# Kernel optimization log

Hardware: AMD Instinct MI355X
Metric: run time of the kernel (lower is better)

Reference implementation:

```python
import jax, jax.numpy as jnp
import numpy as np
from jax import lax

RF, NLF, MESH, FUSION = 64, 16, 16, 64


def _conv3x3(x, w, b):
    # stride 1, pad 1, ksize 3 == SAME
    y = lax.conv_general_dilated(x, w, (1, 1), 'SAME',
                                 dimension_numbers=('NCHW', 'OIHW', 'NCHW'))
    return y + b[None, :, None, None]


def _bn(x, g, b, m, v, eps=1e-5):
    scale = g / jnp.sqrt(v + eps)
    return (x - m[None, :, None, None]) * scale[None, :, None, None] + b[None, :, None, None]


def _rct_block(x, w1, b1, g, be, m, v, w2, b2):
    # extra_conv=True: Conv -> BN -> SiLU -> Conv (all stride 1)
    h = jax.nn.silu(_bn(_conv3x3(x, w1, b1), g, be, m, v))
    return _conv3x3(h, w2, b2)


def setup_inputs():
    key = jax.random.key(0)
    ks = jax.random.split(key, 8)
    B, H, W = 4, 512, 512
    return {
        'feature': jax.random.normal(ks[0], (B, RF, H, W), jnp.float32),
        'p_low': jax.random.normal(ks[1], (B, FUSION, MESH + 1, MESH + 1), jnp.float32),
        'r_w1': jax.random.normal(ks[2], (FUSION, FUSION, 3, 3), jnp.float32) * 0.05,
        'r_b1': jnp.zeros((FUSION,), jnp.float32),
        'r_gamma': jnp.ones((FUSION,), jnp.float32),
        'r_beta': jnp.zeros((FUSION,), jnp.float32),
        'r_mean': jnp.zeros((FUSION,), jnp.float32),
        'r_var': jnp.ones((FUSION,), jnp.float32),
        'r_w2': jax.random.normal(ks[3], (RF * NLF, FUSION, 3, 3), jnp.float32) * 0.05,
        'r_b2': jnp.zeros((RF * NLF,), jnp.float32),
        't_w1': jax.random.normal(ks[4], (FUSION, FUSION, 3, 3), jnp.float32) * 0.05,
        't_b1': jnp.zeros((FUSION,), jnp.float32),
        't_gamma': jnp.ones((FUSION,), jnp.float32),
        't_beta': jnp.zeros((FUSION,), jnp.float32),
        't_mean': jnp.zeros((FUSION,), jnp.float32),
        't_var': jnp.ones((FUSION,), jnp.float32),
        't_w2': jax.random.normal(ks[5], (3 * NLF, FUSION, 3, 3), jnp.float32) * 0.05,
        't_b2': jnp.zeros((3 * NLF,), jnp.float32),
    }


def reference(feature, p_low, r_w1, r_b1, r_gamma, r_beta, r_mean, r_var, r_w2, r_b2,
              t_w1, t_b1, t_gamma, t_beta, t_mean, t_var, t_w2, t_b2):
    B, C, H, W = feature.shape
    M = MESH
    mh, mw = H // M, W // M  # H,W divisible by mesh_size -> pad_tensor is identity
    P = mh * mw

    r_l = _rct_block(p_low, r_w1, r_b1, r_gamma, r_beta, r_mean, r_var, r_w2, r_b2)  # [B, RF*NLF, M+1, M+1]
    t_l = _rct_block(p_low, t_w1, t_b1, t_gamma, t_beta, t_mean, t_var, t_w2, t_b2)  # [B, 3*NLF, M+1, M+1]

    # channel dim factors as (feat, nlf); corners concat along nlf axis in order
    # (i,j), (i,j+1), (i+1,j), (i+1,j+1) -> K = 4*NLF keys per tile
    rc = r_l.reshape(B, RF, NLF, M + 1, M + 1)
    rk = jnp.concatenate([rc[..., :M, :M], rc[..., :M, 1:],
                          rc[..., 1:, :M], rc[..., 1:, 1:]], axis=2)  # [B,RF,4NLF,M,M]
    tc = t_l.reshape(B, 3, NLF, M + 1, M + 1)
    tk = jnp.concatenate([tc[..., :M, :M], tc[..., :M, 1:],
                          tc[..., 1:, :M], tc[..., 1:, 1:]], axis=2)  # [B,3,4NLF,M,M]

    # split feature into tiles: [B, M, M, P, RF] (row-major pixel order within tile)
    f = feature.reshape(B, RF, M, mh, M, mw).transpose(0, 2, 4, 3, 5, 1).reshape(B, M, M, P, RF)

    scale = 1.0 / jnp.sqrt(jnp.float32(RF))
    att = jnp.einsum('bxypr,brkxy->bxypk', f, rk) * scale  # [B,M,M,P,4NLF]
    att = jax.nn.softmax(att, axis=-1)
    out = jnp.einsum('bxypk,bckxy->bxycp', att, tk)  # [B,M,M,3,P]

    Y = out.reshape(B, M, M, 3, mh, mw).transpose(0, 3, 1, 4, 2, 5).reshape(B, 3, H, W)
    return Y
```

## Files before the change

kernel.cpp:

```cpp
#include <hip/hip_runtime.h>

typedef unsigned short u16;
typedef __bf16 bf16x8 __attribute__((ext_vector_type(8)));
typedef unsigned short us8 __attribute__((ext_vector_type(8)));
typedef float f32x4 __attribute__((ext_vector_type(4)));

union U8u { us8 s; u16 u[8]; };

__device__ __forceinline__ u16 f2bf(float f){
  unsigned u = __builtin_bit_cast(unsigned, f);
  u += 0x7fffu + ((u >> 16) & 1u);
  return (u16)(u >> 16);
}
__device__ __forceinline__ bf16x8 asbf(us8 x){ return __builtin_bit_cast(bf16x8, x); }

#define MFMA16(a,b,c) __builtin_amdgcn_mfma_f32_16x16x32_bf16((a),(b),(c),0,0,0)

__device__ __forceinline__ void stage_zero(u16* sS, int tid){
  uint* z = (uint*)sS;
  for (int i = tid; i < 11584; i += 256) z[i] = 0u;
}

__device__ __forceinline__ void stage_src_f32(const float* __restrict__ src,
                                              u16* sS, int tid){
  for (int i4 = tid; i4 < 4624; i4 += 256){
    int e = i4 * 4;
    f32x4 dv = *(const f32x4*)(src + e);
    #pragma unroll
    for (int t = 0; t < 4; t++){
      int ee = e + t;
      int cin = ee / 289; int rr = ee - cin*289;
      int oy = rr / 17;   int ox = rr - oy*17;
      sS[cin*362 + (oy+1)*19 + (ox+1)] = f2bf(dv[t]);
    }
  }
}

__device__ __forceinline__ void stage_src_bf16(const u16* __restrict__ src,
                                               u16* sS, int tid){
  for (int i4 = tid; i4 < 4624; i4 += 256){
    int e = i4 * 4;
    uint2 dv = *(const uint2*)(src + e);
    u16 vv[4] = { (u16)dv.x, (u16)(dv.x >> 16), (u16)dv.y, (u16)(dv.y >> 16) };
    #pragma unroll
    for (int t = 0; t < 4; t++){
      int ee = e + t;
      int cin = ee / 289; int rr = ee - cin*289;
      int oy = rr / 17;   int ox = rr - oy*17;
      sS[cin*362 + (oy+1)*19 + (ox+1)] = vv[t];
    }
  }
}

__device__ __forceinline__ void stage_w_f32(const float* __restrict__ w, int m0,
                                            u16* sW, int tid){
  for (int i4 = tid; i4 < 2304; i4 += 256){
    int e = i4 * 4;
    int co = e / 576; int r0 = e - co*576;
    f32x4 wv = *(const f32x4*)(w + (size_t)(m0+co)*576 + r0);
    #pragma unroll
    for (int t = 0; t < 4; t++){
      int r = r0 + t; int cin = r / 9; int tap = r - cin*9;
      sW[co*584 + tap*64 + cin] = f2bf(wv[t]);
    }
  }
}

__device__ __forceinline__ f32x4 conv_tile(const u16* sS, const u16* sW,
                                           int nt, int l15, int q)
{
  int p = nt*16 + l15; int pc = p > 288 ? 288 : p;
  int oy = pc / 17, ox = pc - oy*17;
  int pb = oy*19 + ox + q*2896;
  f32x4 acc = {0.f, 0.f, 0.f, 0.f};
  #pragma unroll
  for (int ks = 0; ks < 18; ks++){
    const int tap = ks >> 1;
    const int dy = tap / 3, dx = tap - dy*3;
    const int cof = (ks & 1) * 11584 + dy*19 + dx;
    int off = pb + cof;
    U8u bu;
    #pragma unroll
    for (int j = 0; j < 8; j++) bu.u[j] = sS[off + j*362];
    us8 av = *(const us8*)(sW + l15*584 + ks*32 + q*8);
    acc = MFMA16(asbf(av), asbf(bu.s), acc);
  }
  return acc;
}

__global__ __launch_bounds__(256) void conv1_k(
    const float* __restrict__ p_low,
    const float* __restrict__ wR, const float* __restrict__ b1R,
    const float* __restrict__ gR, const float* __restrict__ beR,
    const float* __restrict__ mR, const float* __restrict__ vR,
    const float* __restrict__ wT, const float* __restrict__ b1T,
    const float* __restrict__ gT, const float* __restrict__ beT,
    const float* __restrict__ mT, const float* __restrict__ vT,
    u16* __restrict__ hR, u16* __restrict__ hT)
{
  __shared__ __attribute__((aligned(16))) u16 sS[23168];
  __shared__ __attribute__((aligned(16))) u16 sW[9344];
  int tid = threadIdx.x;
  int bx = blockIdx.x;
  int job = bx >> 4; int rem = bx & 15;
  int b = rem >> 2; int m0 = (rem & 3) << 4;
  const float* w  = job ? wT  : wR;
  const float* b1 = job ? b1T : b1R;
  const float* g  = job ? gT  : gR;
  const float* be = job ? beT : beR;
  const float* mn = job ? mT  : mR;
  const float* vr = job ? vT  : vR;
  u16* out = job ? hT : hR;
  const float* src = p_low + (size_t)b * 18496;

  stage_zero(sS, tid);
  __syncthreads();
  stage_src_f32(src, sS, tid);
  stage_w_f32(w, m0, sW, tid);
  __syncthreads();

  int lane = tid & 63, wave = tid >> 6;
  int l15 = lane & 15, q = lane >> 4;
  float scl[4], sft[4];
  #pragma unroll
  for (int e = 0; e < 4; e++){
    int co = m0 + q*4 + e;
    float s = g[co] / sqrtf(vr[co] + 1e-5f);
    scl[e] = s;
    sft[e] = (b1[co] - mn[co]) * s + be[co];
  }
  for (int nt = wave; nt < 19; nt += 4){
    f32x4 acc = conv_tile(sS, sW, nt, l15, q);
    int p = nt*16 + l15;
    if (p < 289){
      #pragma unroll
      for (int e = 0; e < 4; e++){
        float y = acc[e]*scl[e] + sft[e];
        float si = y / (1.f + __expf(-y));
        out[(size_t)(b*64 + m0 + q*4 + e)*289 + p] = f2bf(si);
      }
    }
  }
}

__global__ __launch_bounds__(256) void conv2_k(
    const u16* __restrict__ hR, const u16* __restrict__ hT,
    const float* __restrict__ w2R, const float* __restrict__ b2R,
    const float* __restrict__ w2T, const float* __restrict__ b2T,
    float* __restrict__ rl, float* __restrict__ tl)
{
  __shared__ __attribute__((aligned(16))) u16 sS[23168];
  __shared__ __attribute__((aligned(16))) u16 sW[9344];
  int tid = threadIdx.x;
  int bx = blockIdx.x;
  const float *w, *bias; const u16* src; float* out;
  int b, m0, Mtot;
  if (bx < 256){
    b = bx >> 6; m0 = (bx & 63) << 4; Mtot = 1024;
    src = hR + (size_t)b*18496; w = w2R; bias = b2R; out = rl;
  } else {
    int i = bx - 256; b = i / 3; int mr = i - b*3; m0 = mr << 4; Mtot = 48;
    src = hT + (size_t)b*18496; w = w2T; bias = b2T; out = tl;
  }

  stage_zero(sS, tid);
  __syncthreads();
  stage_src_bf16(src, sS, tid);
  stage_w_f32(w, m0, sW, tid);
  __syncthreads();

  int lane = tid & 63, wave = tid >> 6;
  int l15 = lane & 15, q = lane >> 4;
  float bs[4];
  #pragma unroll
  for (int e = 0; e < 4; e++) bs[e] = bias[m0 + q*4 + e];
  for (int nt = wave; nt < 19; nt += 4){
    f32x4 acc = conv_tile(sS, sW, nt, l15, q);
    int p = nt*16 + l15;
    if (p < 289){
      #pragma unroll
      for (int e = 0; e < 4; e++)
        out[(size_t)(b*Mtot + m0 + q*4 + e)*289 + p] = acc[e] + bs[e];
    }
  }
}

__global__ __launch_bounds__(256) void attn_k(
    const float* __restrict__ feat,
    const float* __restrict__ rl, const float* __restrict__ tl,
    float* __restrict__ out)
{
  __shared__ __attribute__((aligned(16))) u16 rkT[4608];
  __shared__ float tkF[256];
  int tid = threadIdx.x;
  int ty = blockIdx.x, tx = blockIdx.y, b = blockIdx.z;
  int lane = tid & 63, wave = tid >> 6;
  int l15 = lane & 15, q = lane >> 4;

  #pragma unroll
  for (int it = 0; it < 16; it++){
    int e = tid + it*256;
    int key = e & 63, r = e >> 6;
    int pix = (tx + (key >> 5))*17 + ty + ((key >> 4) & 1);
    float v = rl[(size_t)(b*1024 + r*16 + (key & 15))*289 + pix];
    rkT[key*72 + r] = f2bf(v * 0.125f);
  }
  {
    int c = tid >> 6, key = tid & 63;
    float v = 1.f;
    if (c < 3){
      int pix = (tx + (key >> 5))*17 + ty + ((key >> 4) & 1);
      v = tl[(size_t)(b*48 + c*16 + (key & 15))*289 + pix];
    }
    tkF[c*64 + key] = v;
  }
  __syncthreads();

  bf16x8 frk[4][2];
  #pragma unroll
  for (int nt = 0; nt < 4; nt++)
    #pragma unroll
    for (int ks = 0; ks < 2; ks++)
      frk[nt][ks] = __builtin_bit_cast(bf16x8,
          *(const us8*)(rkT + (nt*16 + l15)*72 + ks*32 + q*8));

  float tkr[4][4];
  #pragma unroll
  for (int c = 0; c < 4; c++)
    #pragma unroll
    for (int nt = 0; nt < 4; nt++)
      tkr[c][nt] = tkF[c*64 + nt*16 + l15];

  const size_t HW = (size_t)512*512;
  for (int cnk = 0; cnk < 16; cnk++){
    int irow = (wave << 3) + (cnk >> 1);
    int j0 = (cnk & 1) << 4;
    int hh = tx*32 + irow;
    const float* fb = feat + ((size_t)b*64 + q*8)*HW + (size_t)hh*512
                           + (ty*32 + j0 + l15);
    U8u a0, a1;
    #pragma unroll
    for (int j = 0; j < 8; j++){
      a0.u[j] = f2bf(fb[(size_t)j*HW]);
      a1.u[j] = f2bf(fb[(size_t)(j+32)*HW]);
    }
    f32x4 acc[4];
    #pragma unroll
    for (int nt = 0; nt < 4; nt++){
      f32x4 zz = {0.f, 0.f, 0.f, 0.f};
      zz = MFMA16(asbf(a0.s), frk[nt][0], zz);
      zz = MFMA16(asbf(a1.s), frk[nt][1], zz);
      acc[nt] = zz;
    }
    #pragma unroll
    for (int nt = 0; nt < 4; nt++)
      #pragma unroll
      for (int e = 0; e < 4; e++)
        acc[nt][e] = __expf(acc[nt][e]);
    float o[4][4];
    #pragma unroll
    for (int c = 0; c < 4; c++)
      #pragma unroll
      for (int e = 0; e < 4; e++)
        o[c][e] = acc[0][e]*tkr[c][0] + acc[1][e]*tkr[c][1]
                + acc[2][e]*tkr[c][2] + acc[3][e]*tkr[c][3];
    #pragma unroll
    for (int mask = 1; mask < 16; mask <<= 1)
      #pragma unroll
      for (int c = 0; c < 4; c++)
        #pragma unroll
        for (int e = 0; e < 4; e++)
          o[c][e] += __shfl_xor(o[c][e], mask, 64);
    if (l15 < 3){
      float i0 = __builtin_amdgcn_rcpf(o[3][0]);
      float i1 = __builtin_amdgcn_rcpf(o[3][1]);
      float i2 = __builtin_amdgcn_rcpf(o[3][2]);
      float i3 = __builtin_amdgcn_rcpf(o[3][3]);
      f32x4 ov;
      ov[0] = o[l15][0]*i0; ov[1] = o[l15][1]*i1;
      ov[2] = o[l15][2]*i2; ov[3] = o[l15][3]*i3;
      *(f32x4*)(out + ((size_t)(b*3 + l15)*512 + hh)*512
                    + (ty*32 + j0 + q*4)) = ov;
    }
  }
}

extern "C" void kernel_launch(void* const* d_in, const int* in_sizes, int n_in,
                              void* d_out, int out_size, void* d_ws, size_t ws_size,
                              hipStream_t stream)
{
  (void)in_sizes; (void)n_in; (void)out_size; (void)ws_size;
  const float* feature = (const float*)d_in[0];
  const float* p_low = (const float*)d_in[1];
  const float* r_w1 = (const float*)d_in[2];
  const float* r_b1 = (const float*)d_in[3];
  const float* r_g  = (const float*)d_in[4];
  const float* r_be = (const float*)d_in[5];
  const float* r_m  = (const float*)d_in[6];
  const float* r_v  = (const float*)d_in[7];
  const float* r_w2 = (const float*)d_in[8];
  const float* r_b2 = (const float*)d_in[9];
  const float* t_w1 = (const float*)d_in[10];
  const float* t_b1 = (const float*)d_in[11];
  const float* t_g  = (const float*)d_in[12];
  const float* t_be = (const float*)d_in[13];
  const float* t_m  = (const float*)d_in[14];
  const float* t_v  = (const float*)d_in[15];
  const float* t_w2 = (const float*)d_in[16];
  const float* t_b2 = (const float*)d_in[17];

  char* ws = (char*)d_ws;
  u16* hR = (u16*)ws;
  u16* hT = hR + (size_t)4*64*289;
  float* rl = (float*)(ws + 295936);
  float* tl = rl + (size_t)4*1024*289;
  float* outp = (float*)d_out;

  hipLaunchKernelGGL(conv1_k, dim3(32), dim3(256), 0, stream,
      p_low, r_w1, r_b1, r_g, r_be, r_m, r_v,
      t_w1, t_b1, t_g, t_be, t_m, t_v, hR, hT);
  hipLaunchKernelGGL(conv2_k, dim3(268), dim3(256), 0, stream,
      hR, hT, r_w2, r_b2, t_w2, t_b2, rl, tl);
  hipLaunchKernelGGL(attn_k, dim3(16, 16, 4), dim3(256), 0, stream,
      feature, rl, tl, outp);
}
```

Measured before the change: 474.5 us.

## Transpose conv staging layout, split conv grids, store keys in bf16, truncate feature

The conv staging buffer becomes pixel-major with channels contiguous, so each MFMA B operand is a single 16-byte LDS load instead of eight scalar loads. Both conv grids are split across pixel tiles to launch more blocks. conv2 now writes pre-scaled bf16 keys and fp32 values in a pixel-major layout, which shrinks the gather traffic in the attention kernel and turns it into vector loads. The attention kernel builds bf16 feature operands with a byte-permute truncation instead of round-to-nearest, which changes rounding slightly.

After: 472.7 us. No clear change (-0.4%).

```diff
diff --git a/kernel.cpp b/kernel.cpp
--- a/kernel.cpp
+++ b/kernel.cpp
@@ -4,6 +4,7 @@
 typedef __bf16 bf16x8 __attribute__((ext_vector_type(8)));
 typedef unsigned short us8 __attribute__((ext_vector_type(8)));
 typedef float f32x4 __attribute__((ext_vector_type(4)));
+typedef unsigned int u32x4 __attribute__((ext_vector_type(4)));
 
 union U8u { us8 s; u16 u[8]; };
 
@@ -16,38 +17,37 @@
 
 #define MFMA16(a,b,c) __builtin_amdgcn_mfma_f32_16x16x32_bf16((a),(b),(c),0,0,0)
 
-__device__ __forceinline__ void stage_zero(u16* sS, int tid){
+__device__ __forceinline__ void stage_zero2(u16* sS, int tid){
   uint* z = (uint*)sS;
-  for (int i = tid; i < 11584; i += 256) z[i] = 0u;
-}
-
-__device__ __forceinline__ void stage_src_f32(const float* __restrict__ src,
-                                              u16* sS, int tid){
+  for (int i = tid; i < 12996; i += 256) z[i] = 0u;
+}
+
+__device__ __forceinline__ void stage_src_f32T(const float* __restrict__ src,
+                                               u16* sS, int tid){
   for (int i4 = tid; i4 < 4624; i4 += 256){
     int e = i4 * 4;
     f32x4 dv = *(const f32x4*)(src + e);
     #pragma unroll
     for (int t = 0; t < 4; t++){
       int ee = e + t;
-      int cin = ee / 289; int rr = ee - cin*289;
-      int oy = rr / 17;   int ox = rr - oy*17;
-      sS[cin*362 + (oy+1)*19 + (ox+1)] = f2bf(dv[t]);
-    }
-  }
-}
-
-__device__ __forceinline__ void stage_src_bf16(const u16* __restrict__ src,
-                                               u16* sS, int tid){
-  for (int i4 = tid; i4 < 4624; i4 += 256){
-    int e = i4 * 4;
-    uint2 dv = *(const uint2*)(src + e);
-    u16 vv[4] = { (u16)dv.x, (u16)(dv.x >> 16), (u16)dv.y, (u16)(dv.y >> 16) };
-    #pragma unroll
-    for (int t = 0; t < 4; t++){
+      int ci = ee / 289; int rr = ee - ci*289;
+      int oy = rr / 17;  int ox = rr - oy*17;
+      sS[((oy+1)*19 + ox+1)*72 + ci] = f2bf(dv[t]);
+    }
+  }
+}
+
+__device__ __forceinline__ void stage_src_bf16T(const u16* __restrict__ src,
+                                                u16* sS, int tid){
+  for (int i8 = tid; i8 < 2312; i8 += 256){
+    int e = i8 * 8;
+    U8u dv; dv.s = *(const us8*)(src + e);
+    #pragma unroll
+    for (int t = 0; t < 8; t++){
       int ee = e + t;
-      int cin = ee / 289; int rr = ee - cin*289;
-      int oy = rr / 17;   int ox = rr - oy*17;
-      sS[cin*362 + (oy+1)*19 + (ox+1)] = vv[t];
+      int ci = ee / 289; int rr = ee - ci*289;
+      int oy = rr / 17;  int ox = rr - oy*17;
+      sS[((oy+1)*19 + ox+1)*72 + ci] = dv.u[t];
     }
   }
 }
@@ -66,24 +66,20 @@
   }
 }
 
-__device__ __forceinline__ f32x4 conv_tile(const u16* sS, const u16* sW,
-                                           int nt, int l15, int q)
+__device__ __forceinline__ f32x4 conv_tile2(const u16* sS, const u16* sW,
+                                            int nt, int l15, int q)
 {
   int p = nt*16 + l15; int pc = p > 288 ? 288 : p;
   int oy = pc / 17, ox = pc - oy*17;
-  int pb = oy*19 + ox + q*2896;
   f32x4 acc = {0.f, 0.f, 0.f, 0.f};
   #pragma unroll
   for (int ks = 0; ks < 18; ks++){
     const int tap = ks >> 1;
     const int dy = tap / 3, dx = tap - dy*3;
-    const int cof = (ks & 1) * 11584 + dy*19 + dx;
-    int off = pb + cof;
-    U8u bu;
-    #pragma unroll
-    for (int j = 0; j < 8; j++) bu.u[j] = sS[off + j*362];
+    int pix2 = (oy+dy)*19 + (ox+dx);
+    us8 bv = *(const us8*)(sS + pix2*72 + (ks & 1)*32 + q*8);
     us8 av = *(const us8*)(sW + l15*584 + ks*32 + q*8);
-    acc = MFMA16(asbf(av), asbf(bu.s), acc);
+    acc = MFMA16(asbf(av), asbf(bv), acc);
   }
   return acc;
 }
@@ -98,12 +94,15 @@
     const float* __restrict__ mT, const float* __restrict__ vT,
     u16* __restrict__ hR, u16* __restrict__ hT)
 {
-  __shared__ __attribute__((aligned(16))) u16 sS[23168];
+  __shared__ __attribute__((aligned(16))) u16 sS[25992];
   __shared__ __attribute__((aligned(16))) u16 sW[9344];
   int tid = threadIdx.x;
   int bx = blockIdx.x;
-  int job = bx >> 4; int rem = bx & 15;
-  int b = rem >> 2; int m0 = (rem & 3) << 4;
+  int job = bx >> 6;
+  int b = (bx >> 4) & 3;
+  int m0 = ((bx >> 2) & 3) << 4;
+  int px = bx & 3;
+  int nt0 = px * 5, ntEnd = nt0 + 5 > 19 ? 19 : nt0 + 5;
   const float* w  = job ? wT  : wR;
   const float* b1 = job ? b1T : b1R;
   const float* g  = job ? gT  : gR;
@@ -113,9 +112,9 @@
   u16* out = job ? hT : hR;
   const float* src = p_low + (size_t)b * 18496;
 
-  stage_zero(sS, tid);
-  __syncthreads();
-  stage_src_f32(src, sS, tid);
+  stage_zero2(sS, tid);
+  __syncthreads();
+  stage_src_f32T(src, sS, tid);
   stage_w_f32(w, m0, sW, tid);
   __syncthreads();
 
@@ -129,8 +128,8 @@
     scl[e] = s;
     sft[e] = (b1[co] - mn[co]) * s + be[co];
   }
-  for (int nt = wave; nt < 19; nt += 4){
-    f32x4 acc = conv_tile(sS, sW, nt, l15, q);
+  for (int nt = nt0 + wave; nt < ntEnd; nt += 4){
+    f32x4 acc = conv_tile2(sS, sW, nt, l15, q);
     int p = nt*16 + l15;
     if (p < 289){
       #pragma unroll
@@ -147,25 +146,28 @@
     const u16* __restrict__ hR, const u16* __restrict__ hT,
     const float* __restrict__ w2R, const float* __restrict__ b2R,
     const float* __restrict__ w2T, const float* __restrict__ b2T,
-    float* __restrict__ rl, float* __restrict__ tl)
-{
-  __shared__ __attribute__((aligned(16))) u16 sS[23168];
+    u16* __restrict__ rlq, float* __restrict__ tlq)
+{
+  __shared__ __attribute__((aligned(16))) u16 sS[25992];
   __shared__ __attribute__((aligned(16))) u16 sW[9344];
   int tid = threadIdx.x;
   int bx = blockIdx.x;
-  const float *w, *bias; const u16* src; float* out;
-  int b, m0, Mtot;
-  if (bx < 256){
-    b = bx >> 6; m0 = (bx & 63) << 4; Mtot = 1024;
-    src = hR + (size_t)b*18496; w = w2R; bias = b2R; out = rl;
+  const float *w, *bias; const u16* src;
+  int b, m0, px, isR;
+  if (bx < 512){
+    isR = 1; b = bx >> 7; int rem = bx & 127;
+    m0 = (rem >> 1) << 4; px = rem & 1;
+    src = hR + (size_t)b*18496; w = w2R; bias = b2R;
   } else {
-    int i = bx - 256; b = i / 3; int mr = i - b*3; m0 = mr << 4; Mtot = 48;
-    src = hT + (size_t)b*18496; w = w2T; bias = b2T; out = tl;
-  }
-
-  stage_zero(sS, tid);
-  __syncthreads();
-  stage_src_bf16(src, sS, tid);
+    isR = 0; int i = bx - 512; b = i / 6; int rr = i - b*6;
+    m0 = (rr >> 1) << 4; px = rr & 1;
+    src = hT + (size_t)b*18496; w = w2T; bias = b2T;
+  }
+  int nt0 = px * 10, ntEnd = px ? 19 : 10;
+
+  stage_zero2(sS, tid);
+  __syncthreads();
+  stage_src_bf16T(src, sS, tid);
   stage_w_f32(w, m0, sW, tid);
   __syncthreads();
 
@@ -174,20 +176,28 @@
   float bs[4];
   #pragma unroll
   for (int e = 0; e < 4; e++) bs[e] = bias[m0 + q*4 + e];
-  for (int nt = wave; nt < 19; nt += 4){
-    f32x4 acc = conv_tile(sS, sW, nt, l15, q);
+  for (int nt = nt0 + wave; nt < ntEnd; nt += 4){
+    f32x4 acc = conv_tile2(sS, sW, nt, l15, q);
     int p = nt*16 + l15;
     if (p < 289){
-      #pragma unroll
-      for (int e = 0; e < 4; e++)
-        out[(size_t)(b*Mtot + m0 + q*4 + e)*289 + p] = acc[e] + bs[e];
+      if (isR){
+        uint2 pk;
+        pk.x = (uint)f2bf((acc[0]+bs[0])*0.125f)
+             | ((uint)f2bf((acc[1]+bs[1])*0.125f) << 16);
+        pk.y = (uint)f2bf((acc[2]+bs[2])*0.125f)
+             | ((uint)f2bf((acc[3]+bs[3])*0.125f) << 16);
+        *(uint2*)(rlq + ((size_t)b*289 + p)*1024 + m0 + q*4) = pk;
+      } else {
+        f32x4 ov = {acc[0]+bs[0], acc[1]+bs[1], acc[2]+bs[2], acc[3]+bs[3]};
+        *(f32x4*)(tlq + ((size_t)b*289 + p)*48 + m0 + q*4) = ov;
+      }
     }
   }
 }
 
 __global__ __launch_bounds__(256) void attn_k(
-    const float* __restrict__ feat,
-    const float* __restrict__ rl, const float* __restrict__ tl,
+    const uint* __restrict__ feat,
+    const u16* __restrict__ rlq, const float* __restrict__ tlq,
     float* __restrict__ out)
 {
   __shared__ __attribute__((aligned(16))) u16 rkT[4608];
@@ -197,22 +207,24 @@
   int lane = tid & 63, wave = tid >> 6;
   int l15 = lane & 15, q = lane >> 4;
 
-  #pragma unroll
-  for (int it = 0; it < 16; it++){
-    int e = tid + it*256;
-    int key = e & 63, r = e >> 6;
-    int pix = (tx + (key >> 5))*17 + ty + ((key >> 4) & 1);
-    float v = rl[(size_t)(b*1024 + r*16 + (key & 15))*289 + pix];
-    rkT[key*72 + r] = f2bf(v * 0.125f);
-  }
   {
-    int c = tid >> 6, key = tid & 63;
-    float v = 1.f;
-    if (c < 3){
-      int pix = (tx + (key >> 5))*17 + ty + ((key >> 4) & 1);
-      v = tl[(size_t)(b*48 + c*16 + (key & 15))*289 + pix];
-    }
-    tkF[c*64 + key] = v;
+    int corner = wave;
+    int pix = (tx + (corner >> 1))*17 + ty + (corner & 1);
+    const u16* sp = rlq + ((size_t)b*289 + pix)*1024 + lane*16;
+    U8u v0, v1; v0.s = *(const us8*)sp; v1.s = *(const us8*)(sp + 8);
+    #pragma unroll
+    for (int nl = 0; nl < 8; nl++){
+      rkT[(corner*16 + nl)*72 + lane]     = v0.u[nl];
+      rkT[(corner*16 + 8 + nl)*72 + lane] = v1.u[nl];
+    }
+  }
+  if (tid < 192){
+    int corner = tid / 48; int idx = tid - corner*48;
+    int pix = (tx + (corner >> 1))*17 + ty + (corner & 1);
+    int c = idx >> 4, nl = idx & 15;
+    tkF[c*64 + corner*16 + nl] = tlq[((size_t)b*289 + pix)*48 + idx];
+  } else {
+    tkF[192 + (tid - 192)] = 1.f;
   }
   __syncthreads();
 
@@ -236,20 +248,29 @@
     int irow = (wave << 3) + (cnk >> 1);
     int j0 = (cnk & 1) << 4;
     int hh = tx*32 + irow;
-    const float* fb = feat + ((size_t)b*64 + q*8)*HW + (size_t)hh*512
-                           + (ty*32 + j0 + l15);
-    U8u a0, a1;
+    const uint* fb = feat + ((size_t)b*64 + q*8)*HW + (size_t)hh*512
+                          + (ty*32 + j0 + l15);
+    uint r0[8], r1[8];
     #pragma unroll
     for (int j = 0; j < 8; j++){
-      a0.u[j] = f2bf(fb[(size_t)j*HW]);
-      a1.u[j] = f2bf(fb[(size_t)(j+32)*HW]);
-    }
+      r0[j] = fb[(size_t)j*HW];
+      r1[j] = fb[(size_t)(j+32)*HW];
+    }
+    u32x4 p0, p1;
+    #pragma unroll
+    for (int j2 = 0; j2 < 4; j2++){
+      p0[j2] = __builtin_amdgcn_perm(r0[2*j2+1], r0[2*j2], 0x07060302u);
+      p1[j2] = __builtin_amdgcn_perm(r1[2*j2+1], r1[2*j2], 0x07060302u);
+    }
+    bf16x8 A0 = __builtin_bit_cast(bf16x8, p0);
+    bf16x8 A1 = __builtin_bit_cast(bf16x8, p1);
+
     f32x4 acc[4];
     #pragma unroll
     for (int nt = 0; nt < 4; nt++){
       f32x4 zz = {0.f, 0.f, 0.f, 0.f};
-      zz = MFMA16(asbf(a0.s), frk[nt][0], zz);
-      zz = MFMA16(asbf(a1.s), frk[nt][1], zz);
+      zz = MFMA16(A0, frk[nt][0], zz);
+      zz = MFMA16(A1, frk[nt][1], zz);
       acc[nt] = zz;
     }
     #pragma unroll
@@ -290,7 +311,7 @@
                               hipStream_t stream)
 {
   (void)in_sizes; (void)n_in; (void)out_size; (void)ws_size;
-  const float* feature = (const float*)d_in[0];
+  const uint*  feature = (const uint*)d_in[0];
   const float* p_low = (const float*)d_in[1];
   const float* r_w1 = (const float*)d_in[2];
   const float* r_b1 = (const float*)d_in[3];
@@ -312,15 +333,15 @@
   char* ws = (char*)d_ws;
   u16* hR = (u16*)ws;
   u16* hT = hR + (size_t)4*64*289;
-  float* rl = (float*)(ws + 295936);
-  float* tl = rl + (size_t)4*1024*289;
+  u16* rlq = (u16*)(ws + 295936);
+  float* tlq = (float*)(ws + 295936 + 2367488);
   float* outp = (float*)d_out;
 
-  hipLaunchKernelGGL(conv1_k, dim3(32), dim3(256), 0, stream,
+  hipLaunchKernelGGL(conv1_k, dim3(128), dim3(256), 0, stream,
       p_low, r_w1, r_b1, r_g, r_be, r_m, r_v,
       t_w1, t_b1, t_g, t_be, t_m, t_v, hR, hT);
-  hipLaunchKernelGGL(conv2_k, dim3(268), dim3(256), 0, stream,
-      hR, hT, r_w2, r_b2, t_w2, t_b2, rl, tl);
+  hipLaunchKernelGGL(conv2_k, dim3(536), dim3(256), 0, stream,
+      hR, hT, r_w2, r_b2, t_w2, t_b2, rlq, tlq);
   hipLaunchKernelGGL(attn_k, dim3(16, 16, 4), dim3(256), 0, stream,
-      feature, rl, tl, outp);
-}
+      feature, rlq, tlq, outp);
+}
```
